# Kernel tuning notes

Measured on AMD Instinct MI355X. Metric: run time of the kernel, lower is better.

Reference implementation:

```python
import jax, jax.numpy as jnp
import numpy as np

D_MODEL = 1024
NUM_HEADS = 16
MAX_LEN = 2048
D_HEAD = D_MODEL // NUM_HEADS
BATCH = 2
SEQ = 2048


def setup_inputs() -> dict:
    key = jax.random.key(0)
    ks = jax.random.split(key, 8)
    s = 1.0 / np.sqrt(D_MODEL)
    return {
        "x": jax.random.normal(ks[0], (BATCH, SEQ, D_MODEL), dtype=jnp.float32),
        "Wq": jax.random.uniform(ks[1], (D_MODEL, D_MODEL), jnp.float32, -s, s),
        "bq": jax.random.uniform(ks[2], (D_MODEL,), jnp.float32, -s, s),
        "Wk": jax.random.uniform(ks[3], (D_MODEL, D_MODEL), jnp.float32, -s, s),
        "bk": jax.random.uniform(ks[4], (D_MODEL,), jnp.float32, -s, s),
        "Wv": jax.random.uniform(ks[5], (D_MODEL, D_MODEL), jnp.float32, -s, s),
        "bv": jax.random.uniform(ks[6], (D_MODEL,), jnp.float32, -s, s),
        "Er": jax.random.normal(ks[7], (MAX_LEN, D_HEAD), dtype=jnp.float32),
    }


def _skew(QEr):
    # QEr: [B, H, S, S]  (music-transformer skew trick)
    B, H, S, _ = QEr.shape
    padded = jnp.pad(QEr, ((0, 0), (0, 0), (0, 0), (1, 0)))  # [B,H,S,S+1]
    reshaped = padded.reshape(B, H, S + 1, S)
    return reshaped[:, :, 1:, :]  # [B,H,S,S]


def reference(x, Wq, bq, Wk, bk, Wv, bv, Er):
    B, S, D = x.shape
    H, Dh = NUM_HEADS, D_HEAD
    # projections (torch Linear: x @ W.T + b)
    q = (jnp.einsum('bsd,ed->bse', x, Wq) + bq).reshape(B, S, H, Dh).transpose(0, 2, 1, 3)
    k = (jnp.einsum('bsd,ed->bse', x, Wk) + bk).reshape(B, S, H, Dh).transpose(0, 2, 1, 3)
    v = (jnp.einsum('bsd,ed->bse', x, Wv) + bv).reshape(B, S, H, Dh).transpose(0, 2, 1, 3)
    # relative position scores
    Er_slice = Er[MAX_LEN - S:, :]                    # [S, Dh]
    QEr = jnp.einsum('bhsd,td->bhst', q, Er_slice)    # [B,H,S,S]
    Srel = _skew(QEr)
    QKt = jnp.einsum('bhsd,bhtd->bhst', q, k)
    attn = (QKt + Srel) / jnp.sqrt(jnp.asarray(Dh, x.dtype))
    causal = jnp.tril(jnp.ones((S, S), dtype=bool))
    attn = jnp.where(causal[None, None], attn, -jnp.inf)
    attn = jax.nn.softmax(attn, axis=-1)
    out = jnp.einsum('bhst,bhtd->bhsd', attn, v)      # [B,H,S,Dh]
    out = out.transpose(0, 2, 1, 3).reshape(B, S, D)
    return out  # dropout is identity in eval mode
```

## Files before the change

### kernel.cpp

```cpp
#include <hip/hip_runtime.h>
#include <hip/hip_bf16.h>

constexpr int B  = 2;
constexpr int S  = 2048;
constexpr int D  = 1024;
constexpr int H  = 16;

typedef unsigned short u16t;
typedef unsigned long long u64;
typedef __attribute__((ext_vector_type(8))) short short8;
typedef __attribute__((ext_vector_type(4))) float float4v;

__device__ __forceinline__ float b2f(unsigned int u) {
    union { unsigned int i; float f; } c; c.i = u << 16; return c.f;
}
__device__ __forceinline__ u16t f2b(float f) {
    __hip_bfloat16 h = __float2bfloat16(f);
    union { __hip_bfloat16 h; u16t u; } c; c.h = h; return c.u;
}
__device__ __forceinline__ int fasi(float f) {
    union { float f; int i; } c; c.f = f; return c.i;
}
__device__ __forceinline__ float iasf(int i) {
    union { int i; float f; } c; c.i = i; return c.f;
}
__device__ __forceinline__ u64 pack4(float4 v) {
    return (u64)f2b(v.x) | ((u64)f2b(v.y) << 16) | ((u64)f2b(v.z) << 32) | ((u64)f2b(v.w) << 48);
}

typedef __attribute__((address_space(1))) const unsigned int* as1_u32p;
typedef __attribute__((address_space(3))) unsigned int* as3_u32p;
__device__ __forceinline__ void gll16(const void* g, void* l) {
    __builtin_amdgcn_global_load_lds((as1_u32p)g, (as3_u32p)l, 16, 0, 0);
}

constexpr size_t XB_OFF = 0;
constexpr size_t WQ_OFF = 4194304;
constexpr size_t WK_OFF = 5242880;
constexpr size_t WV_OFF = 6291456;
constexpr size_t ER_OFF = 7340032;
constexpr size_t QW_OFF = 7471104;
constexpr size_t KW_OFF = 11665408;
constexpr size_t VT_OFF = 15859712;

__global__ __launch_bounds__(256) void prep_bf16(
    const float* __restrict__ x,  const float* __restrict__ Wq,
    const float* __restrict__ Wk, const float* __restrict__ Wv,
    const float* __restrict__ Er, u64* __restrict__ dst)
{
    size_t i4 = (size_t)blockIdx.x * 256 + threadIdx.x;
    const float* src; size_t off;
    if      (i4 < 1048576) { src = x;  off = i4; }
    else if (i4 < 1310720) { src = Wq; off = i4 - 1048576; }
    else if (i4 < 1572864) { src = Wk; off = i4 - 1310720; }
    else if (i4 < 1835008) { src = Wv; off = i4 - 1572864; }
    else                   { src = Er; off = i4 - 1835008; }
    float4 v = ((const float4*)src)[off];
    dst[i4] = pack4(v);
}

__global__ __launch_bounds__(256, 3) void qkv_mfma(
    const u16t* __restrict__ xb,
    const u16t* __restrict__ wqb, const u16t* __restrict__ wkb, const u16t* __restrict__ wvb,
    const float* __restrict__ bq, const float* __restrict__ bk, const float* __restrict__ bv,
    u16t* __restrict__ qo, u16t* __restrict__ ko, u16t* __restrict__ vT)
{
    const int z = blockIdx.z;
    const u16t*  W    = (z == 0) ? wqb : (z == 1) ? wkb : wvb;
    const float* bias = (z == 0) ? bq  : (z == 1) ? bk  : bv;

    __shared__ __align__(16) u16t SMEM[2 * 128 * 64];
    char* XsB = (char*)SMEM;
    char* WsB = XsB + 16384;

    const int tid = threadIdx.x;
    const int w = tid >> 6, lane = tid & 63;
    const int quad = lane >> 4, l16 = lane & 15;
    const int m0 = blockIdx.x * 128, n0 = blockIdx.y * 128;
    const int mi = (w >> 1) * 64, ni = (w & 1) * 64;

    const int srow = lane >> 3;
    const int d8s  = (lane & 7) ^ (srow & 7);
    const int xk   = l16 & 7;

    float4v acc[4][4];
    #pragma unroll
    for (int mt = 0; mt < 4; ++mt)
        #pragma unroll
        for (int nt = 0; nt < 4; ++nt) acc[mt][nt] = (float4v){0.f, 0.f, 0.f, 0.f};

    for (int k0 = 0; k0 < D; k0 += 64) {
        #pragma unroll
        for (int it = 0; it < 4; ++it) {
            int ci  = w * 4 + it;
            int row = ci * 8 + srow;
            gll16(&xb[(size_t)(m0 + row) * D + k0 + d8s * 8], XsB + ci * 1024);
            gll16(&W [(size_t)(n0 + row) * D + k0 + d8s * 8], WsB + ci * 1024);
        }
        __syncthreads();

        short8 af[4][2], bf[4][2];
        #pragma unroll
        for (int mt = 0; mt < 4; ++mt) {
            int r = mi + mt * 16 + l16;
            af[mt][0] = *(const short8*)(XsB + r * 128 + ((quad       ^ xk) << 4));
            af[mt][1] = *(const short8*)(XsB + r * 128 + (((quad + 4) ^ xk) << 4));
        }
        #pragma unroll
        for (int nt = 0; nt < 4; ++nt) {
            int r = ni + nt * 16 + l16;
            bf[nt][0] = *(const short8*)(WsB + r * 128 + ((quad       ^ xk) << 4));
            bf[nt][1] = *(const short8*)(WsB + r * 128 + (((quad + 4) ^ xk) << 4));
        }
        #pragma unroll
        for (int mt = 0; mt < 4; ++mt)
            #pragma unroll
            for (int nt = 0; nt < 4; ++nt) {
                acc[mt][nt] = __builtin_amdgcn_mfma_f32_16x16x32_bf16(af[mt][0], bf[nt][0], acc[mt][nt], 0, 0, 0);
                acc[mt][nt] = __builtin_amdgcn_mfma_f32_16x16x32_bf16(af[mt][1], bf[nt][1], acc[mt][nt], 0, 0, 0);
            }
        __syncthreads();
    }

    float bias_v[4];
    #pragma unroll
    for (int nt = 0; nt < 4; ++nt) bias_v[nt] = bias[n0 + ni + nt * 16 + l16];
    #pragma unroll
    for (int mt = 0; mt < 4; ++mt)
        #pragma unroll
        for (int nt = 0; nt < 4; ++nt)
            #pragma unroll
            for (int rg = 0; rg < 4; ++rg) acc[mt][nt][rg] += bias_v[nt];

    const int hB = n0 >> 6;
    const int b_ = m0 >> 11;
    const int sB = m0 & (S - 1);
    char* EP = (char*)SMEM;

    if (z < 2) {
        u16t* outp = (z == 0) ? qo : ko;
        #pragma unroll 1
        for (int hp = 0; hp < 2; ++hp) {
            __syncthreads();
            if ((w & 1) == hp) {
                #pragma unroll
                for (int mt = 0; mt < 4; ++mt)
                    #pragma unroll
                    for (int nt = 0; nt < 4; ++nt) {
                        int col = nt * 16 + l16;
                        #pragma unroll
                        for (int rg = 0; rg < 4; ++rg) {
                            int row = mi + mt * 16 + quad * 4 + rg;
                            *(u16t*)(EP + row * 144 + col * 2) = f2b(acc[mt][nt][rg]);
                        }
                    }
            }
            __syncthreads();
            #pragma unroll
            for (int it = 0; it < 4; ++it) {
                int idx = tid + it * 256;
                int row = idx >> 3, c8 = idx & 7;
                short8 vv = *(const short8*)(EP + row * 144 + c8 * 16);
                *(short8*)&outp[((size_t)(b_ * H + hB + hp) * S + sB + row) * 64 + c8 * 8] = vv;
            }
        }
    } else {
        #pragma unroll 1
        for (int hp = 0; hp < 2; ++hp) {
            __syncthreads();
            if ((w & 1) == hp) {
                #pragma unroll
                for (int mt = 0; mt < 4; ++mt)
                    #pragma unroll
                    for (int nt = 0; nt < 4; ++nt) {
                        int rowD = nt * 16 + l16;
                        #pragma unroll
                        for (int rg = 0; rg < 4; ++rg) {
                            int colS = mi + mt * 16 + quad * 4 + rg;
                            *(u16t*)(EP + rowD * 272 + colS * 2) = f2b(acc[mt][nt][rg]);
                        }
                    }
            }
            __syncthreads();
            #pragma unroll
            for (int it = 0; it < 4; ++it) {
                int idx = tid + it * 256;
                int rowD = idx >> 4, c16 = idx & 15;
                short8 vv = *(const short8*)(EP + rowD * 272 + c16 * 16);
                *(short8*)&vT[((size_t)(b_ * H + hB + hp) * 64 + rowD) * S + sB + c16 * 8] = vv;
            }
        }
    }
}

__global__ __launch_bounds__(256, 4) void attn_mfma(
    const u16t* __restrict__ q, const u16t* __restrict__ k,
    const u16t* __restrict__ vT, const u16t* __restrict__ er,
    float* __restrict__ out)
{
    __shared__ __align__(16) u16t KsS[2][64 * 64];
    __shared__ __align__(16) u16t VsS[2][64 * 64];
    __shared__ __align__(16) u16t PsS[64 * 64];
    char* KsB = (char*)KsS;
    char* VsB = (char*)VsS;
    char* PsB = (char*)PsS;
    float* lrows = (float*)PsS;

    const int tid = threadIdx.x;
    const int w = tid >> 6, lane = tid & 63;
    const int quad = lane >> 4, l16 = lane & 15;

    const int r_  = blockIdx.x;
    const int g   = blockIdx.y;
    const int bh  = r_ & 31;
    const int slot = r_ >> 5;
    const int ix  = (g == 0) ? (31 - slot)
                  : (g == 1) ? (16 + slot)
                  : (g == 2) ? (15 - slot)
                  :            slot;
    const int hh = bh & (H - 1), bb = bh >> 4;

    const u16t* qb = q  + (size_t)bh * S * 64;
    const u16t* kb = k  + (size_t)bh * S * 64;
    const u16t* vb = vT + (size_t)bh * 64 * S;

    const int xk = (l16 & 7);
    const float SC = 0.18033688f;
    const float M2 = 17.3125f;

    const int srow = lane >> 3;
    const int d8s  = (lane & 7) ^ (srow & 7);

    const int s0 = ix * 64;

    const size_t qoff = (size_t)(s0 + w * 16 + l16) * 64;
    const short8 Qa0 = *(const short8*)&qb[qoff + quad * 8];
    const short8 Qa1 = *(const short8*)&qb[qoff + 32 + quad * 8];

    float4v accO[4], L[5];
    #pragma unroll
    for (int t = 0; t < 4; ++t) accO[t] = (float4v){0.f, 0.f, 0.f, 0.f};
    float lsum[4] = {0.f, 0.f, 0.f, 0.f};

    #pragma unroll
    for (int it = 0; it < 2; ++it) {
        int ci = w * 2 + it;
        int prow = ci * 8 + srow;
        gll16(&kb[(size_t)prow * 64 + d8s * 8], KsB + ci * 1024);
        gll16(&vb[(size_t)prow * S + d8s * 8], VsB + ci * 1024);
    }
    __syncthreads();

    for (int jt = 0; jt <= ix; ++jt) {
        const int t0 = jt * 64;
        const int jbase = S - 64 - s0 + t0;
        const bool diag = (jt == ix);
        const int bsel = (jt & 1) * 8192;

        short8 ef0[4], ef1[4], e00, e01;
        #pragma unroll
        for (int c = 1; c <= 4; ++c) {
            int grow = jbase + (3 - w + c) * 16 + l16;
            if (grow > S - 1) grow = S - 1;
            const u16t* ep = &er[(size_t)grow * 64 + quad * 8];
            ef0[c - 1] = *(const short8*)ep;
            ef1[c - 1] = *(const short8*)(ep + 32);
        }
        if (jt == 0) {
            int grow = jbase + (3 - w) * 16 + l16;
            if (grow > S - 1) grow = S - 1;
            const u16t* ep = &er[(size_t)grow * 64 + quad * 8];
            e00 = *(const short8*)ep;
            e01 = *(const short8*)(ep + 32);
        }

        if (jt < ix) {
            int nb = ((jt + 1) & 1) * 8192;
            #pragma unroll
            for (int it = 0; it < 2; ++it) {
                int ci = w * 2 + it;
                int prow = ci * 8 + srow;
                gll16(&kb[(size_t)(t0 + 64 + prow) * 64 + d8s * 8], KsB + nb + ci * 1024);
                gll16(&vb[(size_t)prow * S + t0 + 64 + d8s * 8], VsB + nb + ci * 1024);
            }
        }

        __builtin_amdgcn_s_setprio(1);
        float4v S1[4];
        #pragma unroll
        for (int nt = 0; nt < 4; ++nt) {
            int row = nt * 16 + l16;
            short8 b0 = *(const short8*)(KsB + bsel + row * 128 + ((quad ^ xk) << 4));
            short8 b1 = *(const short8*)(KsB + bsel + row * 128 + (((quad + 4) ^ xk) << 4));
            float4v a = (float4v){0.f, 0.f, 0.f, 0.f};
            a = __builtin_amdgcn_mfma_f32_16x16x32_bf16(Qa0, b0, a, 0, 0, 0);
            a = __builtin_amdgcn_mfma_f32_16x16x32_bf16(Qa1, b1, a, 0, 0, 0);
            S1[nt] = a;
        }

        if (jt == 0) {
            float4v e = (float4v){0.f, 0.f, 0.f, 0.f};
            e = __builtin_amdgcn_mfma_f32_16x16x32_bf16(Qa0, e00, e, 0, 0, 0);
            e = __builtin_amdgcn_mfma_f32_16x16x32_bf16(Qa1, e01, e, 0, 0, 0);
            L[0] = e;
        } else {
            L[0] = L[4];
        }
        #pragma unroll
        for (int c = 1; c <= 4; ++c) {
            float4v e = (float4v){0.f, 0.f, 0.f, 0.f};
            e = __builtin_amdgcn_mfma_f32_16x16x32_bf16(Qa0, ef0[c - 1], e, 0, 0, 0);
            e = __builtin_amdgcn_mfma_f32_16x16x32_bf16(Qa1, ef1[c - 1], e, 0, 0, 0);
            L[c] = e;
        }
        __builtin_amdgcn_s_setprio(0);

#define SM_BODY(DIAGC)                                                        \
        _Pragma("unroll")                                                     \
        for (int rg = 0; rg < 4; ++rg) {                                      \
            const int usel = quad * 4 + rg;                                   \
            const int thr = 15 - usel;                                        \
            const int sidx = ((lane & 48) | ((l16 + thr) & 15)) * 4;          \
            const bool give_lo = (l16 >= thr);                                \
            int t0v = __builtin_amdgcn_ds_bpermute(sidx, fasi(give_lo ? L[0][rg] : L[1][rg])); \
            int t1v = __builtin_amdgcn_ds_bpermute(sidx, fasi(give_lo ? L[1][rg] : L[2][rg])); \
            int t2v = __builtin_amdgcn_ds_bpermute(sidx, fasi(give_lo ? L[2][rg] : L[3][rg])); \
            int t3v = __builtin_amdgcn_ds_bpermute(sidx, fasi(give_lo ? L[3][rg] : L[4][rg])); \
            float qe[4] = { iasf(t0v), iasf(t1v), iasf(t2v), iasf(t3v) };     \
            const int i_ = w * 16 + usel;                                     \
            const int ikey = i_ & 7;                                          \
            float psum = 0.f;                                                 \
            _Pragma("unroll")                                                 \
            for (int nt = 0; nt < 4; ++nt) {                                  \
                float s2 = fmaf(S1[nt][rg] + qe[nt], SC, -M2);                \
                float p = exp2f(s2);                                          \
                if (DIAGC) p = (nt * 16 + l16 > i_) ? 0.f : p;                \
                psum += p;                                                    \
                int j_ = nt * 16 + l16;                                       \
                *(u16t*)(PsB + i_ * 128 + (((j_ >> 3) ^ ikey) << 4) + (j_ & 7) * 2) = f2b(p); \
            }                                                                 \
            lsum[rg] += psum;                                                 \
        }
        if (diag) { SM_BODY(true) } else { SM_BODY(false) }
#undef SM_BODY

        {
            __builtin_amdgcn_s_setprio(1);
            int ar = w * 16 + l16;
            short8 pa0 = *(const short8*)(PsB + ar * 128 + ((quad ^ (ar & 7)) << 4));
            short8 pa1 = *(const short8*)(PsB + ar * 128 + (((quad + 4) ^ (ar & 7)) << 4));
            #pragma unroll
            for (int td = 0; td < 4; ++td) {
                int row = td * 16 + l16;
                short8 a0 = *(const short8*)(VsB + bsel + row * 128 + ((quad ^ xk) << 4));
                short8 a1 = *(const short8*)(VsB + bsel + row * 128 + (((quad + 4) ^ xk) << 4));
                accO[td] = __builtin_amdgcn_mfma_f32_16x16x32_bf16(a0, pa0, accO[td], 0, 0, 0);
                accO[td] = __builtin_amdgcn_mfma_f32_16x16x32_bf16(a1, pa1, accO[td], 0, 0, 0);
            }
            __builtin_amdgcn_s_setprio(0);
        }
        __syncthreads();
    }

    #pragma unroll
    for (int rg = 0; rg < 4; ++rg) {
        float s = lsum[rg];
        s += __shfl_xor(s, 1);
        s += __shfl_xor(s, 2);
        s += __shfl_xor(s, 4);
        s += __shfl_xor(s, 8);
        if (l16 == 0) lrows[w * 16 + quad * 4 + rg] = s;
    }
    float inv = 1.f / lrows[w * 16 + l16];

    float* ob = out + (size_t)bb * S * D + (size_t)hh * 64
                + (size_t)(s0 + w * 16 + l16) * D;
    #pragma unroll
    for (int td = 0; td < 4; ++td) {
        float4 o;
        o.x = accO[td][0] * inv;
        o.y = accO[td][1] * inv;
        o.z = accO[td][2] * inv;
        o.w = accO[td][3] * inv;
        *(float4*)&ob[td * 16 + quad * 4] = o;
    }
}

extern "C" void kernel_launch(void* const* d_in, const int* in_sizes, int n_in,
                              void* d_out, int out_size, void* d_ws, size_t ws_size,
                              hipStream_t stream) {
    const float* x  = (const float*)d_in[0];
    const float* Wq = (const float*)d_in[1];
    const float* bq = (const float*)d_in[2];
    const float* Wk = (const float*)d_in[3];
    const float* bk = (const float*)d_in[4];
    const float* Wv = (const float*)d_in[5];
    const float* bv = (const float*)d_in[6];
    const float* Er = (const float*)d_in[7];
    float* out = (float*)d_out;

    u16t* ws16 = (u16t*)d_ws;
    u16t* xb  = ws16 + XB_OFF;
    u16t* wqb = ws16 + WQ_OFF;
    u16t* wkb = ws16 + WK_OFF;
    u16t* wvb = ws16 + WV_OFF;
    u16t* erb = ws16 + ER_OFF;
    u16t* qw  = ws16 + QW_OFF;
    u16t* kw  = ws16 + KW_OFF;
    u16t* vTw = ws16 + VT_OFF;

    prep_bf16<<<dim3(7296), dim3(256), 0, stream>>>(x, Wq, Wk, Wv, Er, (u64*)d_ws);

    qkv_mfma<<<dim3(32, 8, 3), dim3(256), 0, stream>>>(
        xb, wqb, wkb, wvb, bq, bk, bv, qw, kw, vTw);

    attn_mfma<<<dim3(256, 4), dim3(256), 0, stream>>>(qw, kw, vTw, erb, out);
}
```

Before: 214.0 us.

## Pack relative-position scores as bf16 pairs for bpermute, add nontemporal stores, drop setprio

The skew shuffle now packs two relative-position logits as bf16 into one 32-bit word, which halves the ds_bpermute count per row group. Intermediate bf16 buffers (prep output, Q/K/V^T) are written with nontemporal stores. The s_setprio hints around the MFMA sections are removed. Rounding the QEr term to bf16 lowers accuracy of the pre-softmax scores, and the nontemporal hint may hurt reuse because the attention kernel reads these buffers right after they are written.

```diff
diff --git a/kernel.cpp b/kernel.cpp
--- a/kernel.cpp
+++ b/kernel.cpp
@@ -18,11 +18,8 @@
     __hip_bfloat16 h = __float2bfloat16(f);
     union { __hip_bfloat16 h; u16t u; } c; c.h = h; return c.u;
 }
-__device__ __forceinline__ int fasi(float f) {
-    union { float f; int i; } c; c.f = f; return c.i;
-}
-__device__ __forceinline__ float iasf(int i) {
-    union { int i; float f; } c; c.i = i; return c.f;
+__device__ __forceinline__ unsigned int pkbf(float a, float b) {
+    return (unsigned int)f2b(a) | ((unsigned int)f2b(b) << 16);
 }
 __device__ __forceinline__ u64 pack4(float4 v) {
     return (u64)f2b(v.x) | ((u64)f2b(v.y) << 16) | ((u64)f2b(v.z) << 32) | ((u64)f2b(v.w) << 48);
@@ -56,7 +53,7 @@
     else if (i4 < 1835008) { src = Wv; off = i4 - 1572864; }
     else                   { src = Er; off = i4 - 1835008; }
     float4 v = ((const float4*)src)[off];
-    dst[i4] = pack4(v);
+    __builtin_nontemporal_store(pack4(v), &dst[i4]);
 }
 
 __global__ __launch_bounds__(256, 3) void qkv_mfma(
@@ -161,7 +158,8 @@
                 int idx = tid + it * 256;
                 int row = idx >> 3, c8 = idx & 7;
                 short8 vv = *(const short8*)(EP + row * 144 + c8 * 16);
-                *(short8*)&outp[((size_t)(b_ * H + hB + hp) * S + sB + row) * 64 + c8 * 8] = vv;
+                __builtin_nontemporal_store(vv,
+                    (short8*)&outp[((size_t)(b_ * H + hB + hp) * S + sB + row) * 64 + c8 * 8]);
             }
         }
     } else {
@@ -187,7 +185,8 @@
                 int idx = tid + it * 256;
                 int rowD = idx >> 4, c16 = idx & 15;
                 short8 vv = *(const short8*)(EP + rowD * 272 + c16 * 16);
-                *(short8*)&vT[((size_t)(b_ * H + hB + hp) * 64 + rowD) * S + sB + c16 * 8] = vv;
+                __builtin_nontemporal_store(vv,
+                    (short8*)&vT[((size_t)(b_ * H + hB + hp) * 64 + rowD) * S + sB + c16 * 8]);
             }
         }
     }
@@ -285,7 +284,6 @@
             }
         }
 
-        __builtin_amdgcn_s_setprio(1);
         float4v S1[4];
         #pragma unroll
         for (int nt = 0; nt < 4; ++nt) {
@@ -313,7 +311,6 @@
             e = __builtin_amdgcn_mfma_f32_16x16x32_bf16(Qa1, ef1[c - 1], e, 0, 0, 0);
             L[c] = e;
         }
-        __builtin_amdgcn_s_setprio(0);
 
 #define SM_BODY(DIAGC)                                                        \
         _Pragma("unroll")                                                     \
@@ -322,11 +319,12 @@
             const int thr = 15 - usel;                                        \
             const int sidx = ((lane & 48) | ((l16 + thr) & 15)) * 4;          \
             const bool give_lo = (l16 >= thr);                                \
-            int t0v = __builtin_amdgcn_ds_bpermute(sidx, fasi(give_lo ? L[0][rg] : L[1][rg])); \
-            int t1v = __builtin_amdgcn_ds_bpermute(sidx, fasi(give_lo ? L[1][rg] : L[2][rg])); \
-            int t2v = __builtin_amdgcn_ds_bpermute(sidx, fasi(give_lo ? L[2][rg] : L[3][rg])); \
-            int t3v = __builtin_amdgcn_ds_bpermute(sidx, fasi(give_lo ? L[3][rg] : L[4][rg])); \
-            float qe[4] = { iasf(t0v), iasf(t1v), iasf(t2v), iasf(t3v) };     \
+            unsigned int p01 = give_lo ? pkbf(L[0][rg], L[1][rg]) : pkbf(L[1][rg], L[2][rg]); \
+            unsigned int p23 = give_lo ? pkbf(L[2][rg], L[3][rg]) : pkbf(L[3][rg], L[4][rg]); \
+            unsigned int q01 = (unsigned int)__builtin_amdgcn_ds_bpermute(sidx, (int)p01); \
+            unsigned int q23 = (unsigned int)__builtin_amdgcn_ds_bpermute(sidx, (int)p23); \
+            float qe[4] = { b2f(q01 & 0xffffu), b2f(q01 >> 16),               \
+                            b2f(q23 & 0xffffu), b2f(q23 >> 16) };             \
             const int i_ = w * 16 + usel;                                     \
             const int ikey = i_ & 7;                                          \
             float psum = 0.f;                                                 \
@@ -345,7 +343,6 @@
 #undef SM_BODY
 
         {
-            __builtin_amdgcn_s_setprio(1);
             int ar = w * 16 + l16;
             short8 pa0 = *(const short8*)(PsB + ar * 128 + ((quad ^ (ar & 7)) << 4));
             short8 pa1 = *(const short8*)(PsB + ar * 128 + (((quad + 4) ^ (ar & 7)) << 4));
@@ -357,7 +354,6 @@
                 accO[td] = __builtin_amdgcn_mfma_f32_16x16x32_bf16(a0, pa0, accO[td], 0, 0, 0);
                 accO[td] = __builtin_amdgcn_mfma_f32_16x16x32_bf16(a1, pa1, accO[td], 0, 0, 0);
             }
-            __builtin_amdgcn_s_setprio(0);
         }
         __syncthreads();
     }
```

Result: slower. 237.6 us (+11.1%).
